# Performance work log

Measured on AMD Instinct MI355X. Metric: run time of the kernel, lower is better.

Reference implementation:

```python
import jax, jax.numpy as jnp
import numpy as np

DIM = 4096
KROT = 8
GROUP = 128
NG = DIM // GROUP  # 32 groups
N = 16384          # tokens


def setup_inputs() -> dict:
    key = jax.random.key(0)
    kx, kt, ks = jax.random.split(key, 3)
    x = jax.random.normal(kx, (N, DIM), dtype=jnp.float32)
    theta = jax.random.normal(kt, (KROT, DIM // 2), dtype=jnp.float32) * 0.1
    # pairs: for each krot layer, a permutation of [0, GROUP) tiled across groups
    rng = np.random.default_rng(0)
    pairs = np.stack([
        np.tile(rng.permutation(GROUP).astype(np.int32), NG) for _ in range(KROT)
    ])  # [KROT, DIM], local (within-group) indices
    channel_scales = jax.random.uniform(ks, (1, DIM), dtype=jnp.float32,
                                        minval=0.5, maxval=1.5)
    return {"x": x, "pairs": jnp.asarray(pairs), "theta": theta,
            "channel_scales": channel_scales}


def reference(x, pairs, theta, channel_scales):
    # global channel offset for each position of the tiled permutation
    off = jnp.repeat(jnp.arange(NG, dtype=jnp.int32) * GROUP, GROUP)  # [DIM]
    for k in range(KROT):
        idx = pairs[k] + off          # [DIM] global channel indices (a permutation)
        ie = idx[0::2]                # [DIM//2] first element of each Givens pair
        io = idx[1::2]                # [DIM//2] second element
        a = x[:, ie]                  # [N, DIM//2]
        b = x[:, io]
        c = jnp.cos(theta[k])         # [DIM//2]
        s = jnp.sin(theta[k])
        x = x.at[:, ie].set(a * c - b * s).at[:, io].set(a * s + b * c)
    return x * channel_scales
```

## Files before the change

kernel.cpp:

```cpp
#include <hip/hip_runtime.h>

#define DIMX   4096
#define KROT   8
#define GROUPC 128
#define NGG    32
#define NROWS  16384
#define RPT    128
#define NTASKS (NGG * (NROWS / RPT))


__global__ void rot_setup(const float* __restrict__ theta,
                          const int* __restrict__ pairs,
                          float* __restrict__ cs, int* __restrict__ ao) {
    int i = blockIdx.x * 256 + threadIdx.x;
    if (i < KROT * (DIMX / 2)) {
        float t = theta[i];
        cs[2 * i]     = cosf(t);
        cs[2 * i + 1] = sinf(t);
    }
    if (i < KROT * 64) {
        int k = i >> 6, p = i & 63;
        int ie = pairs[k * DIMX + 2 * p];
        int io = pairs[k * DIMX + 2 * p + 1];
        ao[2 * i]     = (ie << 9) | (((ie >> 1) & 31) << 3);
        ao[2 * i + 1] = (io << 9) | (((io >> 1) & 31) << 3);
    }
}

__global__ __launch_bounds__(256) void rot_main(
    const float* __restrict__ x, const float* __restrict__ scales,
    const float* __restrict__ cs, const int* __restrict__ ao,
    float* __restrict__ out) {
    __shared__ float lds[RPT * GROUPC];
    const int tid  = threadIdx.x;
    const int lane = tid & 63;
    const int wave = tid >> 6;
    const int c    = lane * 2;
    const int eb   = (lane & 31) << 1;
    const int wbase = __builtin_amdgcn_readfirstlane(wave * 16);
    char* lp = (char*)lds;

    for (int task = blockIdx.x; task < NTASKS; task += gridDim.x) {
        const int rowblock = task >> 5;
        const int g        = task & 31;
        const float* xb = x   + (size_t)rowblock * RPT * DIMX + g * GROUPC;
        float*       ob = out + (size_t)rowblock * RPT * DIMX + g * GROUPC;

        __syncthreads();

        #pragma unroll 8
        for (int it = 0; it < RPT / 4; ++it) {
            int t = it * 4 + wave;
            float2 v = *(const float2*)(xb + (size_t)t * DIMX + c);
            int slot = t ^ eb;
            lds[c * RPT + slot]       = v.x;
            lds[(c + 1) * RPT + slot] = v.y;
        }
        __syncthreads();

        for (int k = 0; k < KROT; ++k) {
            const float* csb = cs + ((k * 2048 + g * 64) << 1);
            const int*   aob = ao + (k << 7);
            #pragma unroll
            for (int i = 0; i < 16; ++i) {
                int p = wbase + i;
                int2   A = *(const int2*)(aob + 2 * p);
                float2 w = *(const float2*)(csb + 2 * p);
                float2 a = *(float2*)(lp + (A.x ^ (lane << 3)));
                float2 b = *(float2*)(lp + (A.y ^ (lane << 3)));
                float2 na, nb;
                na.x = a.x * w.x - b.x * w.y;
                na.y = a.y * w.x - b.y * w.y;
                nb.x = a.x * w.y + b.x * w.x;
                nb.y = a.y * w.y + b.y * w.x;
                *(float2*)(lp + (A.x ^ (lane << 3))) = na;
                *(float2*)(lp + (A.y ^ (lane << 3))) = nb;
            }
            __syncthreads();
        }

        float2 sc = *(const float2*)(scales + g * GROUPC + c);
        #pragma unroll 8
        for (int it = 0; it < RPT / 4; ++it) {
            int t = it * 4 + wave;
            int slot = t ^ eb;
            float2 v;
            v.x = lds[c * RPT + slot]       * sc.x;
            v.y = lds[(c + 1) * RPT + slot] * sc.y;
            *(float2*)(ob + (size_t)t * DIMX + c) = v;
        }
    }
}

extern "C" void kernel_launch(void* const* d_in, const int* in_sizes, int n_in,
                              void* d_out, int out_size, void* d_ws, size_t ws_size,
                              hipStream_t stream) {
    const float* x      = (const float*)d_in[0];
    const int*   pairs  = (const int*)d_in[1];
    const float* theta  = (const float*)d_in[2];
    const float* scales = (const float*)d_in[3];
    float* outp = (float*)d_out;

    float* cs = (float*)d_ws;
    int*   ao = (int*)((char*)d_ws + (size_t)2 * KROT * 2048 * sizeof(float));

    rot_setup<<<64, 256, 0, stream>>>(theta, pairs, cs, ao);
    rot_main<<<512, 256, 0, stream>>>(x, scales, cs, ao, outp);
}
```

Before: 474.1 us.

## Compose Givens rotations into per-group matrix and apply via split-bf16 MFMA GEMM

```diff
diff --git a/kernel.cpp b/kernel.cpp
--- a/kernel.cpp
+++ b/kernel.cpp
@@ -1,109 +1,153 @@
 #include <hip/hip_runtime.h>
+#include <hip/hip_bf16.h>
 
-#define DIMX   4096
-#define KROT   8
-#define GROUPC 128
-#define NGG    32
-#define NROWS  16384
-#define RPT    128
-#define NTASKS (NGG * (NROWS / RPT))
+#define DIMX  4096
+#define KROT  8
+#define GRP   128
+#define NGG   32
+#define NROWS 16384
+#define RTILE 128
+#define NRT   (NROWS / RTILE)
+#define PBLK  16
 
+typedef float f32x4 __attribute__((ext_vector_type(4)));
+typedef short s16x8 __attribute__((ext_vector_type(8)));
+typedef unsigned short u16;
 
-__global__ void rot_setup(const float* __restrict__ theta,
-                          const int* __restrict__ pairs,
-                          float* __restrict__ cs, int* __restrict__ ao) {
-    int i = blockIdx.x * 256 + threadIdx.x;
-    if (i < KROT * (DIMX / 2)) {
-        float t = theta[i];
-        cs[2 * i]     = cosf(t);
-        cs[2 * i + 1] = sinf(t);
+__global__ __launch_bounds__(512) void compose(const float* __restrict__ theta,
+                                               const int*   __restrict__ pairs,
+                                               const float* __restrict__ scales,
+                                               u16* __restrict__ B) {
+    __shared__ float M[GRP * GRP];
+    const int g = blockIdx.x;
+    const int tid = threadIdx.x;
+    const int j = tid & 127, q = tid >> 7;
+
+    for (int r = q * 32; r < q * 32 + 32; ++r) M[r * GRP + j] = (r == j) ? 1.f : 0.f;
+    __syncthreads();
+
+    for (int k = 0; k < KROT; ++k) {
+        for (int t = 0; t < 16; ++t) {
+            int tp = q * 16 + t;
+            int ie = pairs[k * DIMX + g * GRP + 2 * tp];
+            int io = pairs[k * DIMX + g * GRP + 2 * tp + 1];
+            float ang = theta[k * (DIMX / 2) + g * 64 + tp];
+            float c = cosf(ang), s = sinf(ang);
+            float a = M[ie * GRP + j], b = M[io * GRP + j];
+            M[ie * GRP + j] = a * c - b * s;
+            M[io * GRP + j] = a * s + b * c;
+        }
+        __syncthreads();
     }
-    if (i < KROT * 64) {
-        int k = i >> 6, p = i & 63;
-        int ie = pairs[k * DIMX + 2 * p];
-        int io = pairs[k * DIMX + 2 * p + 1];
-        ao[2 * i]     = (ie << 9) | (((ie >> 1) & 31) << 3);
-        ao[2 * i + 1] = (io << 9) | (((io >> 1) & 31) << 3);
+
+    const int l = tid & 63, nt = (tid >> 6) & 1, ks = (tid >> 7) & 3;
+    for (int w = 0; w < 4; ++w) {
+        int c = w * 32 + nt * 16 + (l & 15);
+        float sc = scales[g * GRP + c];
+        int dbase = ks * 32 + ((l >> 4) & 3) * 8;
+        s16x8 vh, vl;
+        #pragma unroll
+        for (int e = 0; e < 8; ++e) {
+            float v = sc * M[c * GRP + dbase + e];
+            __hip_bfloat16 h = __float2bfloat16(v);
+            float r = v - __bfloat162float(h);
+            __hip_bfloat16 lo = __float2bfloat16(r);
+            vh[e] = (short)*(u16*)&h;
+            vl[e] = (short)*(u16*)&lo;
+        }
+        int off = (((g * 4 + w) * 4 + ks) * 2 + nt) * 2;
+        *(s16x8*)(B + (size_t)(off + 0) * 512 + l * 8) = vh;
+        *(s16x8*)(B + (size_t)(off + 1) * 512 + l * 8) = vl;
     }
 }
 
-__global__ __launch_bounds__(256) void rot_main(
-    const float* __restrict__ x, const float* __restrict__ scales,
-    const float* __restrict__ cs, const int* __restrict__ ao,
-    float* __restrict__ out) {
-    __shared__ float lds[RPT * GROUPC];
-    const int tid  = threadIdx.x;
-    const int lane = tid & 63;
-    const int wave = tid >> 6;
-    const int c    = lane * 2;
-    const int eb   = (lane & 31) << 1;
-    const int wbase = __builtin_amdgcn_readfirstlane(wave * 16);
-    char* lp = (char*)lds;
+__global__ __launch_bounds__(256, 2) void rot_gemm(const float* __restrict__ x,
+                                                   const u16* __restrict__ B,
+                                                   float* __restrict__ out) {
+    __shared__ float At[RTILE * GRP];
+    const int tid = threadIdx.x;
+    const int l = tid & 63, wv = tid >> 6;
+    const int g = blockIdx.x >> 4;
+    const int p = blockIdx.x & (PBLK - 1);
 
-    for (int task = blockIdx.x; task < NTASKS; task += gridDim.x) {
-        const int rowblock = task >> 5;
-        const int g        = task & 31;
-        const float* xb = x   + (size_t)rowblock * RPT * DIMX + g * GROUPC;
-        float*       ob = out + (size_t)rowblock * RPT * DIMX + g * GROUPC;
+    s16x8 bh[4][2], bl[4][2];
+    #pragma unroll
+    for (int ks = 0; ks < 4; ++ks)
+        #pragma unroll
+        for (int nt = 0; nt < 2; ++nt) {
+            int off = (((g * 4 + wv) * 4 + ks) * 2 + nt) * 2;
+            bh[ks][nt] = *(const s16x8*)(B + (size_t)(off + 0) * 512 + l * 8);
+            bl[ks][nt] = *(const s16x8*)(B + (size_t)(off + 1) * 512 + l * 8);
+        }
 
-        __syncthreads();
+    for (int t = p; t < NRT; t += PBLK) {
+        const float* xb = x + (size_t)t * RTILE * DIMX + g * GRP;
 
-        #pragma unroll 8
-        for (int it = 0; it < RPT / 4; ++it) {
-            int t = it * 4 + wave;
-            float2 v = *(const float2*)(xb + (size_t)t * DIMX + c);
-            int slot = t ^ eb;
-            lds[c * RPT + slot]       = v.x;
-            lds[(c + 1) * RPT + slot] = v.y;
+        #pragma unroll
+        for (int i = 0; i < 16; ++i) {
+            int Lb = i * 256 + tid;
+            int row = Lb >> 5, blk = Lb & 31;
+            const float* src = xb + (size_t)row * DIMX + ((blk ^ (row & 7)) * 4);
+            float* dst = &At[(i * 256 + wv * 64) * 4];
+            __builtin_amdgcn_global_load_lds(
+                (const __attribute__((address_space(1))) void*)src,
+                (__attribute__((address_space(3))) void*)dst, 16, 0, 0);
         }
         __syncthreads();
 
-        for (int k = 0; k < KROT; ++k) {
-            const float* csb = cs + ((k * 2048 + g * 64) << 1);
-            const int*   aob = ao + (k << 7);
+        f32x4 acc[8][2] = {};
+        #pragma unroll
+        for (int ks = 0; ks < 4; ++ks) {
             #pragma unroll
-            for (int i = 0; i < 16; ++i) {
-                int p = wbase + i;
-                int2   A = *(const int2*)(aob + 2 * p);
-                float2 w = *(const float2*)(csb + 2 * p);
-                float2 a = *(float2*)(lp + (A.x ^ (lane << 3)));
-                float2 b = *(float2*)(lp + (A.y ^ (lane << 3)));
-                float2 na, nb;
-                na.x = a.x * w.x - b.x * w.y;
-                na.y = a.y * w.x - b.y * w.y;
-                nb.x = a.x * w.y + b.x * w.x;
-                nb.y = a.y * w.y + b.y * w.x;
-                *(float2*)(lp + (A.x ^ (lane << 3))) = na;
-                *(float2*)(lp + (A.y ^ (lane << 3))) = nb;
+            for (int m = 0; m < 8; ++m) {
+                int row = m * 16 + (l & 15);
+                int bb = ks * 8 + ((l >> 4) & 3) * 2;
+                const f32x4* lp = (const f32x4*)At;
+                f32x4 a0 = lp[row * 32 + ((bb)     ^ (row & 7))];
+                f32x4 a1 = lp[row * 32 + ((bb + 1) ^ (row & 7))];
+                s16x8 ah, al;
+                #pragma unroll
+                for (int e = 0; e < 8; ++e) {
+                    float v = (e < 4) ? a0[e] : a1[e - 4];
+                    __hip_bfloat16 h = __float2bfloat16(v);
+                    float rr = v - __bfloat162float(h);
+                    __hip_bfloat16 lo = __float2bfloat16(rr);
+                    ah[e] = (short)*(u16*)&h;
+                    al[e] = (short)*(u16*)&lo;
+                }
+                #pragma unroll
+                for (int nt = 0; nt < 2; ++nt) {
+                    acc[m][nt] = __builtin_amdgcn_mfma_f32_16x16x32_bf16(ah, bh[ks][nt], acc[m][nt], 0, 0, 0);
+                    acc[m][nt] = __builtin_amdgcn_mfma_f32_16x16x32_bf16(ah, bl[ks][nt], acc[m][nt], 0, 0, 0);
+                    acc[m][nt] = __builtin_amdgcn_mfma_f32_16x16x32_bf16(al, bh[ks][nt], acc[m][nt], 0, 0, 0);
+                }
             }
-            __syncthreads();
         }
+        __syncthreads();
 
-        float2 sc = *(const float2*)(scales + g * GROUPC + c);
-        #pragma unroll 8
-        for (int it = 0; it < RPT / 4; ++it) {
-            int t = it * 4 + wave;
-            int slot = t ^ eb;
-            float2 v;
-            v.x = lds[c * RPT + slot]       * sc.x;
-            v.y = lds[(c + 1) * RPT + slot] * sc.y;
-            *(float2*)(ob + (size_t)t * DIMX + c) = v;
-        }
+        float* ob = out + (size_t)t * RTILE * DIMX + g * GRP + wv * 32;
+        #pragma unroll
+        for (int m = 0; m < 8; ++m)
+            #pragma unroll
+            for (int nt = 0; nt < 2; ++nt)
+                #pragma unroll
+                for (int i = 0; i < 4; ++i) {
+                    int row = m * 16 + ((l >> 4) & 3) * 4 + i;
+                    ob[(size_t)row * DIMX + nt * 16 + (l & 15)] = acc[m][nt][i];
+                }
     }
 }
 
 extern "C" void kernel_launch(void* const* d_in, const int* in_sizes, int n_in,
                               void* d_out, int out_size, void* d_ws, size_t ws_size,
                               hipStream_t stream) {
-    const float* x      = (const float*)d_in[0];
+    const float* xin    = (const float*)d_in[0];
     const int*   pairs  = (const int*)d_in[1];
     const float* theta  = (const float*)d_in[2];
     const float* scales = (const float*)d_in[3];
     float* outp = (float*)d_out;
+    u16*   Btab = (u16*)d_ws;
 
-    float* cs = (float*)d_ws;
-    int*   ao = (int*)((char*)d_ws + (size_t)2 * KROT * 2048 * sizeof(float));
-
-    rot_setup<<<64, 256, 0, stream>>>(theta, pairs, cs, ao);
-    rot_main<<<512, 256, 0, stream>>>(x, scales, cs, ao, outp);
+    compose<<<NGG, 512, 0, stream>>>(theta, pairs, scales, Btab);
+    rot_gemm<<<NGG * PBLK, 256, 0, stream>>>(xin, Btab, outp);
 }
```

Result: slower. 544.4 us (+14.8%).
